# Kernel optimization log

Measured on AMD Instinct MI355X. Metric: run time of the kernel, lower is better.

The kernel has to match this reference:

```python
import jax, jax.numpy as jnp
import numpy as np

THRESHOLD = 0.4
MARGIN = 1.0
EPS = 1e-8  # torch F.cosine_similarity norm clamp


def setup_inputs() -> dict:
    key = jax.random.key(0)
    ks = jax.random.split(key, 8)
    B, N, D, T = 4096, 200000, 256, 10
    h_graph = jax.random.normal(ks[0], (B, D), jnp.float32)
    h_sub = jax.random.normal(ks[1], (N, D), jnp.float32)
    sub2graph = jax.random.randint(ks[2], (N,), 0, B, dtype=jnp.int32)
    W1 = jax.random.normal(ks[3], (D, 2 * D), jnp.float32) / np.float32(np.sqrt(D))
    b1 = jnp.zeros((2 * D,), jnp.float32)
    W2 = jax.random.normal(ks[4], (2 * D, 1), jnp.float32) / np.float32(np.sqrt(2 * D))
    b2 = jnp.zeros((1,), jnp.float32)
    Wc = jax.random.normal(ks[5], (2 * D, T), jnp.float32) / np.float32(np.sqrt(2 * D))
    bc = jnp.zeros((T,), jnp.float32)
    return dict(h_graph=h_graph, h_sub=h_sub, W1=W1, b1=b1, W2=W2, b2=b2,
                Wc=Wc, bc=bc, sub2graph=sub2graph)


def _forward(h_graph, h_sub, W1, b1, W2, b2, Wc, bc, sub2graph):
    B = h_graph.shape[0]
    dt = h_sub.dtype
    # SubMaskGenerator: Linear -> ReLU -> (Dropout off, eval) -> Linear -> sigmoid
    subgraph_mask = jax.nn.sigmoid((jax.nn.relu(h_sub @ W1 + b1) @ W2 + b2)[:, 0])  # [N]
    valid = (subgraph_mask > THRESHOLD).astype(dt)               # mask > threshold
    envm = (subgraph_mask <= THRESHOLD - 0.1).astype(dt)         # mask <= threshold-0.1
    # threshold-masked per-graph mean scatter (aggr='mean')
    sum_v = jax.ops.segment_sum(h_sub * valid[:, None], sub2graph, num_segments=B)
    cnt_v = jax.ops.segment_sum(valid, sub2graph, num_segments=B)
    h_sub_aligned = sum_v / jnp.maximum(cnt_v, 1.0)[:, None]     # zeros when no valid subs
    sum_e = jax.ops.segment_sum(h_sub * envm[:, None], sub2graph, num_segments=B)
    cnt_e = jax.ops.segment_sum(envm, sub2graph, num_segments=B)
    h_sub_env = sum_e / jnp.maximum(cnt_e, 1.0)[:, None]
    # pairwise cosine distances (norms clamped like torch)
    an = jnp.maximum(jnp.linalg.norm(h_sub_aligned, axis=-1), EPS)  # [B]
    en = jnp.maximum(jnp.linalg.norm(h_sub_env, axis=-1), EPS)      # [B]
    pos_d = 1.0 - (h_sub_aligned @ h_sub_aligned.T) / (an[:, None] * an[None, :])  # [B,B]
    neg_d = 1.0 - (h_sub_aligned @ h_sub_env.T) / (an[:, None] * en[None, :])      # [B,B]
    nz_pos = jnp.any(h_sub_aligned != 0, axis=1)
    nz_neg = jnp.any(h_sub_env != 0, axis=1)
    pos_num = jnp.maximum(nz_pos.sum() - 1, 1).astype(dt)
    num_env = nz_neg.sum()
    negative = (neg_d * nz_neg[None, :].astype(dt)).sum(1) / jnp.maximum(num_env, 1).astype(dt)
    positive = pos_d.sum(1) / pos_num
    contrib = jax.nn.relu(positive - negative + MARGIN) * nz_pos.astype(dt) * (num_env > 0).astype(dt)
    contrastive_loss = contrib.sum() / B
    out = jnp.concatenate([h_graph, h_sub_aligned], axis=1) @ Wc + bc
    return out, contrastive_loss, subgraph_mask


def reference(h_graph, h_sub, W1, b1, W2, b2, Wc, bc, sub2graph):
    return _forward(h_graph, h_sub, W1, b1, W2, b2, Wc, bc, sub2graph)
```

## Files before the change

kernel.cpp:

```cpp
#include <hip/hip_runtime.h>

#define N_SUB 200000
#define N_GR  4096
#define DIM   256
#define HID   512
#define TCLS  10
#define MROWS 64
#define RCAP  16384
#define RMARG 1e-3f
#define NREP  128

typedef __attribute__((ext_vector_type(8))) short short8;
typedef __attribute__((ext_vector_type(4))) float f32x4;

__device__ __forceinline__ short bf16_rne(float x){
  unsigned u = __builtin_bit_cast(unsigned, x);
  unsigned r = (u + 0x7FFFu + ((u >> 16) & 1u)) >> 16;
  return (short)r;
}
__device__ __forceinline__ float bf16_to_f(short h){
  unsigned u = ((unsigned)(unsigned short)h) << 16;
  return __builtin_bit_cast(float, u);
}
__device__ __forceinline__ float wave_reduce(float v){
  #pragma unroll
  for (int d = 1; d < 64; d <<= 1) v += __shfl_xor(v, d, 64);
  return v;
}
__device__ __forceinline__ int a_gran(int mt, int mrow, int ks, int kgrp){
  return (((((mt*8 + ks)*4 + kgrp)*2 + (mrow>>3)) << 3)
          | ((mrow & 7) ^ ((ks & 3) << 1) ^ (kgrp & 1)));
}

__global__ __launch_bounds__(256) void bconv_kernel(const float* __restrict__ W1,
                                                    short* __restrict__ bth,
                                                    short* __restrict__ btl,
                                                    int* cnt_all, float* S32, float* Se32,
                                                    float* S, float* Se,
                                                    int* counters, float* loss_p, int* rcnt){
  const int i = blockIdx.x*256 + threadIdx.x;
  if (i < N_GR) cnt_all[i] = 0;
  if (i < NREP*DIM){ S32[i] = 0.f; Se32[i] = 0.f; }
  if (i < DIM){ S[i] = 0.f; Se[i] = 0.f; }
  if (i < 64) loss_p[i] = 0.f;
  if (i < 2) counters[i] = 0;
  if (i == 0) rcnt[0] = 0;
  const int k = i >> 9;
  const int j = i & 511;
  const float x = W1[i];
  const short h = bf16_rne(x);
  const short l = bf16_rne(x - bf16_to_f(h));
  const int nt = j >> 4, mrow = j & 15;
  const int ksg = k >> 5, kgrp = (k >> 3) & 3, kk = k & 7;
  const int lane = kgrp*16 + mrow;
  const size_t dst = (((size_t)(nt*8 + ksg)*64 + lane) << 3) + kk;
  bth[dst] = h;
  btl[dst] = l;
}

__global__ __launch_bounds__(1024) void mask_gemm(
    const float* __restrict__ hsub, const short* __restrict__ bth,
    const short* __restrict__ btl, const float* __restrict__ b1,
    const float* __restrict__ W2, const float* __restrict__ b2,
    const int* __restrict__ s2g, float* __restrict__ mask_out,
    int* __restrict__ cnt_all, int* __restrict__ rlist, int* __restrict__ rcnt)
{
  __shared__ short a_hi[16384];
  __shared__ short a_lo[16384];
  __shared__ float sred[1024];
  const int tid = threadIdx.x;
  const int lane = tid & 63;
  const int c = tid >> 6;
  const int mrow = lane & 15;
  const int kgrp = lane >> 4;
  const int brow = blockIdx.x*MROWS;

  f32x4 acc[4][2];
  #pragma unroll
  for (int mt=0; mt<4; ++mt)
    #pragma unroll
    for (int nt=0; nt<2; ++nt) acc[mt][nt] = (f32x4){0.f,0.f,0.f,0.f};

  const float* __restrict__ gbase = hsub + (size_t)brow*DIM;
  {
    float4 g[4];
    #pragma unroll
    for (int i = 0; i < 4; ++i){
      const int idx = i*1024 + tid;
      g[i] = *reinterpret_cast<const float4*>(gbase + (size_t)idx*4);
    }
    #pragma unroll
    for (int i = 0; i < 4; ++i){
      const int idx = i*1024 + tid;
      const int rr = idx >> 6;
      const int ch = idx & 63;
      const float4 v = g[i];
      const short h0=bf16_rne(v.x), h1=bf16_rne(v.y), h2=bf16_rne(v.z), h3=bf16_rne(v.w);
      const short l0=bf16_rne(v.x-bf16_to_f(h0)), l1=bf16_rne(v.y-bf16_to_f(h1));
      const short l2=bf16_rne(v.z-bf16_to_f(h2)), l3=bf16_rne(v.w-bf16_to_f(h3));
      const int so = a_gran(rr>>4, rr&15, ch>>3, (ch>>1)&3)*8 + (ch&1)*4;
      *reinterpret_cast<short4*>(&a_hi[so]) = make_short4(h0,h1,h2,h3);
      *reinterpret_cast<short4*>(&a_lo[so]) = make_short4(l0,l1,l2,l3);
    }
  }
  __syncthreads();

  short8 Ah[4], Al[4];
  #pragma unroll
  for (int ks = 0; ks < 8; ++ks){
    #pragma unroll
    for (int m = 0; m < 4; ++m){
      const int so = a_gran(m, mrow, ks, kgrp)*8;
      Ah[m] = *reinterpret_cast<const short8*>(&a_hi[so]);
      Al[m] = *reinterpret_cast<const short8*>(&a_lo[so]);
    }
    #pragma unroll
    for (int nt = 0; nt < 2; ++nt){
      const int ntg = c*2 + nt;
      const size_t bo = (((size_t)(ntg*8 + ks)*64 + lane) << 3);
      const short8 Bh = *reinterpret_cast<const short8*>(bth + bo);
      const short8 Bl = *reinterpret_cast<const short8*>(btl + bo);
      #pragma unroll
      for (int m = 0; m < 4; ++m){
        acc[m][nt] = __builtin_amdgcn_mfma_f32_16x16x32_bf16(Ah[m], Bh, acc[m][nt], 0,0,0);
        acc[m][nt] = __builtin_amdgcn_mfma_f32_16x16x32_bf16(Ah[m], Bl, acc[m][nt], 0,0,0);
        acc[m][nt] = __builtin_amdgcn_mfma_f32_16x16x32_bf16(Al[m], Bh, acc[m][nt], 0,0,0);
      }
    }
  }

  float w2v[2], b1v[2];
  #pragma unroll
  for (int nt=0; nt<2; ++nt){
    const int n = c*32 + nt*16 + mrow;
    w2v[nt] = W2[n]; b1v[nt] = b1[n];
  }
  #pragma unroll
  for (int mt=0; mt<4; ++mt){
    #pragma unroll
    for (int r=0; r<4; ++r){
      float s = 0.f;
      #pragma unroll
      for (int nt=0; nt<2; ++nt)
        s += fmaxf(acc[mt][nt][r] + b1v[nt], 0.f) * w2v[nt];
      s += __shfl_xor(s, 1, 64);
      s += __shfl_xor(s, 2, 64);
      s += __shfl_xor(s, 4, 64);
      s += __shfl_xor(s, 8, 64);
      if (mrow == 0)
        sred[c*64 + mt*16 + kgrp*4 + r] = s;
    }
  }
  __syncthreads();
  if (tid < MROWS){
    const int rr = brow + tid;
    float tot = b2[0];
    #pragma unroll
    for (int w = 0; w < 16; ++w) tot += sred[w*64 + tid];
    const float m = 1.f / (1.f + expf(-tot));
    mask_out[rr] = m;
    atomicAdd(&cnt_all[s2g[rr]], 1);
    if (fabsf(m - 0.4f) < RMARG || fabsf(m - 0.3f) < RMARG){
      const int p = atomicAdd(rcnt, 1);
      if (p < RCAP) rlist[p] = rr;
    }
  }
}

__global__ __launch_bounds__(512) void refine_kernel(
    const float* __restrict__ hsub, const float* __restrict__ W1,
    const float* __restrict__ b1, const float* __restrict__ W2,
    const float* __restrict__ b2, const int* __restrict__ rlist,
    const int* __restrict__ rcnt, float* __restrict__ mask_out)
{
  __shared__ float arow[256];
  __shared__ float red[512];
  const int n = min(rcnt[0], RCAP);
  const int t = threadIdx.x;
  for (int it = blockIdx.x; it < n; it += gridDim.x){
    const int row = rlist[it];
    if (t < 256) arow[t] = hsub[(size_t)row*DIM + t];
    __syncthreads();
    float y0 = b1[t], y1 = 0.f, y2 = 0.f, y3 = 0.f;
    #pragma unroll 8
    for (int k = 0; k < 64; ++k){
      y0 = fmaf(arow[k],     W1[(size_t)k*512 + t],         y0);
      y1 = fmaf(arow[k+64],  W1[(size_t)(k+64)*512 + t],    y1);
      y2 = fmaf(arow[k+128], W1[(size_t)(k+128)*512 + t],   y2);
      y3 = fmaf(arow[k+192], W1[(size_t)(k+192)*512 + t],   y3);
    }
    const float y = (y0 + y1) + (y2 + y3);
    red[t] = fmaxf(y, 0.f) * W2[t];
    __syncthreads();
    #pragma unroll
    for (int off = 256; off > 0; off >>= 1){
      if (t < off) red[t] += red[t+off];
      __syncthreads();
    }
    if (t == 0) mask_out[row] = 1.f / (1.f + expf(-(red[0] + b2[0])));
    __syncthreads();
  }
}

__global__ __launch_bounds__(1024) void scan_kernel(const int* __restrict__ cnt,
                                                    int* __restrict__ offs,
                                                    int* __restrict__ cursor){
  __shared__ int buf[1024];
  const int t = threadIdx.x;
  const int c0 = cnt[t*4], c1 = cnt[t*4+1], c2 = cnt[t*4+2], c3 = cnt[t*4+3];
  const int s = c0+c1+c2+c3;
  buf[t] = s; __syncthreads();
  for (int d = 1; d < 1024; d <<= 1){
    int v = (t >= d) ? buf[t-d] : 0;
    __syncthreads();
    buf[t] += v;
    __syncthreads();
  }
  const int excl = buf[t] - s;
  const int o0 = excl, o1 = excl+c0, o2 = o1+c1, o3 = o2+c2;
  offs[t*4]=o0; offs[t*4+1]=o1; offs[t*4+2]=o2; offs[t*4+3]=o3;
  cursor[t*4]=o0; cursor[t*4+1]=o1; cursor[t*4+2]=o2; cursor[t*4+3]=o3;
  if (t == 1023) offs[4096] = buf[1023];
}

__global__ void fill_kernel(const int* __restrict__ s2g, int* __restrict__ cursor,
                            int* __restrict__ list){
  const int i = blockIdx.x*blockDim.x + threadIdx.x;
  if (i < N_SUB){
    const int g = s2g[i];
    const int p = atomicAdd(&cursor[g], 1);
    list[p] = i;
  }
}

__global__ __launch_bounds__(256) void graph_means(
    const float* __restrict__ hsub, const float* __restrict__ mask,
    const int* __restrict__ list, const int* __restrict__ offs,
    const float* __restrict__ hgraph, const float* __restrict__ Wc,
    const float* __restrict__ bc, unsigned short* __restrict__ hatAb,
    float* __restrict__ S32, float* __restrict__ Se32,
    int* __restrict__ nzflags, int* __restrict__ counters,
    float* __restrict__ out)
{
  __shared__ int   sidx[256];
  __shared__ unsigned char sflag[256];
  __shared__ float wr4[4][4];
  __shared__ float wrc[TCLS][4];
  const int g = blockIdx.x;
  const int t = threadIdx.x;
  const int w = t >> 6, lane = t & 63;
  const int start = offs[g], end = offs[g+1];
  const int cnt = end - start;
  float sv = 0.f, sev = 0.f;
  int cv = 0, ce = 0;
  for (int base = 0; base < cnt; base += 256){
    const int nb = min(256, cnt - base);
    __syncthreads();
    if (t < nb){
      const int i = list[start + base + t];
      sidx[t] = i;
      const float m = mask[i];
      sflag[t] = (m > 0.4f) ? 1 : ((m <= 0.3f) ? 2 : 0);
    }
    __syncthreads();
    for (int p = 0; p < nb; p += 4){
      const int lim = nb - p;
      const int i0 = sidx[p];
      const int i1 = (lim > 1) ? sidx[p+1] : i0;
      const int i2 = (lim > 2) ? sidx[p+2] : i0;
      const int i3 = (lim > 3) ? sidx[p+3] : i0;
      const int f0 = sflag[p];
      const int f1 = (lim > 1) ? sflag[p+1] : 0;
      const int f2 = (lim > 2) ? sflag[p+2] : 0;
      const int f3 = (lim > 3) ? sflag[p+3] : 0;
      const float v0 = hsub[(size_t)i0*DIM + t];
      const float v1 = hsub[(size_t)i1*DIM + t];
      const float v2 = hsub[(size_t)i2*DIM + t];
      const float v3 = hsub[(size_t)i3*DIM + t];
      if (f0==1){ sv+=v0; cv++; } else if (f0==2){ sev+=v0; ce++; }
      if (f1==1){ sv+=v1; cv++; } else if (f1==2){ sev+=v1; ce++; }
      if (f2==1){ sv+=v2; cv++; } else if (f2==2){ sev+=v2; ce++; }
      if (f3==1){ sv+=v3; cv++; } else if (f3==2){ sev+=v3; ce++; }
    }
  }
  __syncthreads();
  const float aligned = sv  / fmaxf((float)cv, 1.f);
  const float envv    = sev / fmaxf((float)ce, 1.f);
  float r0 = wave_reduce(aligned*aligned);
  float r1 = wave_reduce(envv*envv);
  float r2 = wave_reduce(aligned != 0.f ? 1.f : 0.f);
  float r3 = wave_reduce(envv    != 0.f ? 1.f : 0.f);
  if (lane == 0){ wr4[w][0]=r0; wr4[w][1]=r1; wr4[w][2]=r2; wr4[w][3]=r3; }
  __syncthreads();
  const float an2  = wr4[0][0]+wr4[1][0]+wr4[2][0]+wr4[3][0];
  const float en2  = wr4[0][1]+wr4[1][1]+wr4[2][1]+wr4[3][1];
  const float nzpf = wr4[0][2]+wr4[1][2]+wr4[2][2]+wr4[3][2];
  const float nzef = wr4[0][3]+wr4[1][3]+wr4[2][3]+wr4[3][3];
  const bool nzp = nzpf > 0.f, nze = nzef > 0.f;
  const float an = fmaxf(sqrtf(an2), 1e-8f);
  const float en = fmaxf(sqrtf(en2), 1e-8f);
  const float ha = aligned / an;
  hatAb[(size_t)g*DIM + t] = (unsigned short)bf16_rne(ha);
  atomicAdd(&S32[((g & (NREP-1)) << 8) + t], ha);
  if (nze) atomicAdd(&Se32[((g & (NREP-1)) << 8) + t], envv / en);
  if (t == 0){
    nzflags[g] = nzp ? 1 : 0;
    if (nzp) atomicAdd(&counters[0], 1);
    if (nze) atomicAdd(&counters[1], 1);
  }
  const float hg = hgraph[(size_t)g*DIM + t];
  #pragma unroll
  for (int c = 0; c < TCLS; ++c){
    float part = hg*Wc[t*TCLS+c] + aligned*Wc[(DIM+t)*TCLS+c];
    part = wave_reduce(part);
    if (lane == 0) wrc[c][w] = part;
  }
  __syncthreads();
  if (t < TCLS)
    out[g*TCLS + t] = wrc[t][0]+wrc[t][1]+wrc[t][2]+wrc[t][3] + bc[t];
}

__global__ __launch_bounds__(256) void combine_kernel(const float* __restrict__ S32,
                                                      const float* __restrict__ Se32,
                                                      float* __restrict__ S,
                                                      float* __restrict__ Se){
  const int b = blockIdx.x;
  const int t = threadIdx.x;
  float s = 0.f, se = 0.f;
  #pragma unroll
  for (int r = 0; r < 8; ++r){
    s  += S32[(b*8 + r)*DIM + t];
    se += Se32[(b*8 + r)*DIM + t];
  }
  atomicAdd(&S[t], s);
  atomicAdd(&Se[t], se);
}

__global__ __launch_bounds__(256) void loss_kernel(
    const unsigned short* __restrict__ hatAb, const float* __restrict__ S,
    const float* __restrict__ Se, const int* __restrict__ nzflags,
    const int* __restrict__ counters, float* __restrict__ loss_p)
{
  __shared__ float wr[4][2];
  const int g = blockIdx.x, t = threadIdx.x;
  const int w = t >> 6, lane = t & 63;
  const float ha = bf16_to_f((short)hatAb[(size_t)g*DIM + t]);
  float p0 = wave_reduce(ha*S[t]);
  float p1 = wave_reduce(ha*Se[t]);
  if (lane == 0){ wr[w][0] = p0; wr[w][1] = p1; }
  __syncthreads();
  if (t == 0){
    const float dS  = wr[0][0]+wr[1][0]+wr[2][0]+wr[3][0];
    const float dSe = wr[0][1]+wr[1][1]+wr[2][1]+wr[3][1];
    const int nzp_cnt = counters[0];
    const int nenv = counters[1];
    const float pos_num = fmaxf((float)(nzp_cnt - 1), 1.f);
    const float positive = (4096.f - dS) / pos_num;
    const float negative = ((float)nenv - dSe) / fmaxf((float)nenv, 1.f);
    float contrib = fmaxf(positive - negative + 1.f, 0.f);
    contrib *= (nzflags[g] ? 1.f : 0.f) * ((nenv > 0) ? 1.f : 0.f);
    atomicAdd(&loss_p[g & 63], contrib * (1.f/4096.f));
  }
}

__global__ void final_loss(const float* __restrict__ loss_p, float* __restrict__ loss){
  const int t = threadIdx.x;
  float v = loss_p[t];
  v = wave_reduce(v);
  if (t == 0) loss[0] = v;
}

extern "C" void kernel_launch(void* const* d_in, const int* in_sizes, int n_in,
                              void* d_out, int out_size, void* d_ws, size_t ws_size,
                              hipStream_t stream) {
  const float* h_graph = (const float*)d_in[0];
  const float* h_sub   = (const float*)d_in[1];
  const float* W1      = (const float*)d_in[2];
  const float* b1      = (const float*)d_in[3];
  const float* W2      = (const float*)d_in[4];
  const float* b2      = (const float*)d_in[5];
  const float* Wc      = (const float*)d_in[6];
  const float* bc      = (const float*)d_in[7];
  const int*   s2g     = (const int*)d_in[8];

  float* out  = (float*)d_out;
  float* loss = out + N_GR*TCLS;
  float* mask = loss + 1;

  char* ws = (char*)d_ws;
  short* bth    = (short*)ws;
  short* btl    = bth + HID*DIM;
  unsigned short* hatAb = (unsigned short*)(btl + HID*DIM);
  int* cnt_all  = (int*)(hatAb + (size_t)N_GR*DIM);
  int* offs     = cnt_all + N_GR;
  int* cursor   = offs + N_GR + 1;
  int* list     = cursor + N_GR;
  int* nzflags  = list + N_SUB;
  int* counters = nzflags + N_GR;
  int* rcnt     = counters + 2;
  int* rlist    = rcnt + 1;
  float* S      = (float*)(rlist + RCAP);
  float* Se     = S + DIM;
  float* S32    = Se + DIM;
  float* Se32   = S32 + NREP*DIM;
  float* loss_p = Se32 + NREP*DIM;

  hipLaunchKernelGGL(bconv_kernel, dim3(HID*DIM/256), dim3(256), 0, stream,
                     W1, bth, btl, cnt_all, S32, Se32, S, Se, counters, loss_p, rcnt);
  hipLaunchKernelGGL(mask_gemm, dim3(N_SUB/MROWS), dim3(1024), 0, stream,
                     h_sub, bth, btl, b1, W2, b2, s2g, mask, cnt_all, rlist, rcnt);
  hipLaunchKernelGGL(refine_kernel, dim3(384), dim3(512), 0, stream,
                     h_sub, W1, b1, W2, b2, rlist, rcnt, mask);
  hipLaunchKernelGGL(scan_kernel, dim3(1), dim3(1024), 0, stream,
                     cnt_all, offs, cursor);
  hipLaunchKernelGGL(fill_kernel, dim3((N_SUB+255)/256), dim3(256), 0, stream,
                     s2g, cursor, list);
  hipLaunchKernelGGL(graph_means, dim3(N_GR), dim3(256), 0, stream,
                     h_sub, mask, list, offs, h_graph, Wc, bc,
                     hatAb, S32, Se32, nzflags, counters, out);
  hipLaunchKernelGGL(combine_kernel, dim3(16), dim3(256), 0, stream,
                     S32, Se32, S, Se);
  hipLaunchKernelGGL(loss_kernel, dim3(N_GR), dim3(256), 0, stream,
                     hatAb, S, Se, nzflags, counters, loss_p);
  hipLaunchKernelGGL(final_loss, dim3(1), dim3(64), 0, stream,
                     loss_p, loss);
}
```

Baseline: 398.2 us.

## Process two row tiles per mask_gemm block with prefetched second-tile loads

Each mask_gemm block now handles two 64-row tiles. Global loads for both tiles are issued up front, so the second tile's fetch overlaps the first tile's conversion, MFMA work and epilogue. The aim is to hide HBM latency and halve the block count, at the cost of holding extra registers for the prefetched data and serialising the two tiles within a block. Bounds clamping is added for the odd final tile.

Result: slower. 408.5 us (+2.6%).

```diff
diff --git a/kernel.cpp b/kernel.cpp
--- a/kernel.cpp
+++ b/kernel.cpp
@@ -73,98 +73,123 @@
   const int c = tid >> 6;
   const int mrow = lane & 15;
   const int kgrp = lane >> 4;
-  const int brow = blockIdx.x*MROWS;
+  const int brow1 = blockIdx.x*(2*MROWS);
+  const int brow2 = brow1 + MROWS;
 
   f32x4 acc[4][2];
+
+#define CONVERT(G)                                                            \
+  { _Pragma("unroll")                                                         \
+    for (int i = 0; i < 4; ++i){                                              \
+      const int idx = i*1024 + tid;                                           \
+      const int rr = idx >> 6;                                                \
+      const int ch = idx & 63;                                                \
+      const float4 v = G[i];                                                  \
+      const short h0=bf16_rne(v.x), h1=bf16_rne(v.y), h2=bf16_rne(v.z), h3=bf16_rne(v.w); \
+      const short l0=bf16_rne(v.x-bf16_to_f(h0)), l1=bf16_rne(v.y-bf16_to_f(h1)); \
+      const short l2=bf16_rne(v.z-bf16_to_f(h2)), l3=bf16_rne(v.w-bf16_to_f(h3)); \
+      const int so = a_gran(rr>>4, rr&15, ch>>3, (ch>>1)&3)*8 + (ch&1)*4;     \
+      *reinterpret_cast<short4*>(&a_hi[so]) = make_short4(h0,h1,h2,h3);       \
+      *reinterpret_cast<short4*>(&a_lo[so]) = make_short4(l0,l1,l2,l3);       \
+    } }
+
+#define KSLOOP                                                                \
+  { short8 Ah[4], Al[4];                                                      \
+    _Pragma("unroll")                                                         \
+    for (int ks = 0; ks < 8; ++ks){                                           \
+      _Pragma("unroll")                                                       \
+      for (int m = 0; m < 4; ++m){                                            \
+        const int so = a_gran(m, mrow, ks, kgrp)*8;                           \
+        Ah[m] = *reinterpret_cast<const short8*>(&a_hi[so]);                  \
+        Al[m] = *reinterpret_cast<const short8*>(&a_lo[so]);                  \
+      }                                                                       \
+      _Pragma("unroll")                                                       \
+      for (int nt = 0; nt < 2; ++nt){                                         \
+        const int ntg = c*2 + nt;                                             \
+        const size_t bo = (((size_t)(ntg*8 + ks)*64 + lane) << 3);            \
+        const short8 Bh = *reinterpret_cast<const short8*>(bth + bo);         \
+        const short8 Bl = *reinterpret_cast<const short8*>(btl + bo);         \
+        _Pragma("unroll")                                                     \
+        for (int m = 0; m < 4; ++m){                                          \
+          acc[m][nt] = __builtin_amdgcn_mfma_f32_16x16x32_bf16(Ah[m], Bh, acc[m][nt], 0,0,0); \
+          acc[m][nt] = __builtin_amdgcn_mfma_f32_16x16x32_bf16(Ah[m], Bl, acc[m][nt], 0,0,0); \
+          acc[m][nt] = __builtin_amdgcn_mfma_f32_16x16x32_bf16(Al[m], Bh, acc[m][nt], 0,0,0); \
+        } } } }
+
+#define EPILOGUE(BROW)                                                        \
+  { float w2v[2], b1v[2];                                                     \
+    _Pragma("unroll")                                                         \
+    for (int nt=0; nt<2; ++nt){                                               \
+      const int n = c*32 + nt*16 + mrow;                                      \
+      w2v[nt] = W2[n]; b1v[nt] = b1[n];                                       \
+    }                                                                         \
+    _Pragma("unroll")                                                         \
+    for (int mt=0; mt<4; ++mt){                                               \
+      _Pragma("unroll")                                                       \
+      for (int r=0; r<4; ++r){                                                \
+        float s = 0.f;                                                        \
+        _Pragma("unroll")                                                     \
+        for (int nt=0; nt<2; ++nt)                                            \
+          s += fmaxf(acc[mt][nt][r] + b1v[nt], 0.f) * w2v[nt];                \
+        s += __shfl_xor(s, 1, 64);                                            \
+        s += __shfl_xor(s, 2, 64);                                            \
+        s += __shfl_xor(s, 4, 64);                                            \
+        s += __shfl_xor(s, 8, 64);                                            \
+        if (mrow == 0)                                                        \
+          sred[c*64 + mt*16 + kgrp*4 + r] = s;                                \
+      } }                                                                     \
+    __syncthreads();                                                          \
+    if (tid < MROWS){                                                         \
+      const int rr = (BROW) + tid;                                            \
+      if (rr < N_SUB){                                                        \
+        float tot = b2[0];                                                    \
+        _Pragma("unroll")                                                     \
+        for (int w = 0; w < 16; ++w) tot += sred[w*64 + tid];                 \
+        const float m = 1.f / (1.f + expf(-tot));                             \
+        mask_out[rr] = m;                                                     \
+        atomicAdd(&cnt_all[s2g[rr]], 1);                                      \
+        if (fabsf(m - 0.4f) < RMARG || fabsf(m - 0.3f) < RMARG){              \
+          const int p = atomicAdd(rcnt, 1);                                   \
+          if (p < RCAP) rlist[p] = rr;                                        \
+        }                                                                     \
+      } } }
+
+  float4 g1[4], g2[4];
+  #pragma unroll
+  for (int i = 0; i < 4; ++i){
+    const int idx = i*1024 + tid;
+    g1[i] = *reinterpret_cast<const float4*>(hsub + (size_t)(brow1 + (idx>>6))*DIM + (idx&63)*4);
+  }
+  #pragma unroll
+  for (int i = 0; i < 4; ++i){
+    const int idx = i*1024 + tid;
+    const int rg = min(brow2 + (idx>>6), N_SUB-1);
+    g2[i] = *reinterpret_cast<const float4*>(hsub + (size_t)rg*DIM + (idx&63)*4);
+  }
+
   #pragma unroll
   for (int mt=0; mt<4; ++mt)
     #pragma unroll
     for (int nt=0; nt<2; ++nt) acc[mt][nt] = (f32x4){0.f,0.f,0.f,0.f};
-
-  const float* __restrict__ gbase = hsub + (size_t)brow*DIM;
-  {
-    float4 g[4];
+  CONVERT(g1);
+  __syncthreads();
+  KSLOOP;
+  EPILOGUE(brow1);
+  __syncthreads();
+
+  if (brow2 < N_SUB){
     #pragma unroll
-    for (int i = 0; i < 4; ++i){
-      const int idx = i*1024 + tid;
-      g[i] = *reinterpret_cast<const float4*>(gbase + (size_t)idx*4);
-    }
-    #pragma unroll
-    for (int i = 0; i < 4; ++i){
-      const int idx = i*1024 + tid;
-      const int rr = idx >> 6;
-      const int ch = idx & 63;
-      const float4 v = g[i];
-      const short h0=bf16_rne(v.x), h1=bf16_rne(v.y), h2=bf16_rne(v.z), h3=bf16_rne(v.w);
-      const short l0=bf16_rne(v.x-bf16_to_f(h0)), l1=bf16_rne(v.y-bf16_to_f(h1));
-      const short l2=bf16_rne(v.z-bf16_to_f(h2)), l3=bf16_rne(v.w-bf16_to_f(h3));
-      const int so = a_gran(rr>>4, rr&15, ch>>3, (ch>>1)&3)*8 + (ch&1)*4;
-      *reinterpret_cast<short4*>(&a_hi[so]) = make_short4(h0,h1,h2,h3);
-      *reinterpret_cast<short4*>(&a_lo[so]) = make_short4(l0,l1,l2,l3);
-    }
-  }
-  __syncthreads();
-
-  short8 Ah[4], Al[4];
-  #pragma unroll
-  for (int ks = 0; ks < 8; ++ks){
-    #pragma unroll
-    for (int m = 0; m < 4; ++m){
-      const int so = a_gran(m, mrow, ks, kgrp)*8;
-      Ah[m] = *reinterpret_cast<const short8*>(&a_hi[so]);
-      Al[m] = *reinterpret_cast<const short8*>(&a_lo[so]);
-    }
-    #pragma unroll
-    for (int nt = 0; nt < 2; ++nt){
-      const int ntg = c*2 + nt;
-      const size_t bo = (((size_t)(ntg*8 + ks)*64 + lane) << 3);
-      const short8 Bh = *reinterpret_cast<const short8*>(bth + bo);
-      const short8 Bl = *reinterpret_cast<const short8*>(btl + bo);
+    for (int mt=0; mt<4; ++mt)
       #pragma unroll
-      for (int m = 0; m < 4; ++m){
-        acc[m][nt] = __builtin_amdgcn_mfma_f32_16x16x32_bf16(Ah[m], Bh, acc[m][nt], 0,0,0);
-        acc[m][nt] = __builtin_amdgcn_mfma_f32_16x16x32_bf16(Ah[m], Bl, acc[m][nt], 0,0,0);
-        acc[m][nt] = __builtin_amdgcn_mfma_f32_16x16x32_bf16(Al[m], Bh, acc[m][nt], 0,0,0);
-      }
-    }
-  }
-
-  float w2v[2], b1v[2];
-  #pragma unroll
-  for (int nt=0; nt<2; ++nt){
-    const int n = c*32 + nt*16 + mrow;
-    w2v[nt] = W2[n]; b1v[nt] = b1[n];
-  }
-  #pragma unroll
-  for (int mt=0; mt<4; ++mt){
-    #pragma unroll
-    for (int r=0; r<4; ++r){
-      float s = 0.f;
-      #pragma unroll
-      for (int nt=0; nt<2; ++nt)
-        s += fmaxf(acc[mt][nt][r] + b1v[nt], 0.f) * w2v[nt];
-      s += __shfl_xor(s, 1, 64);
-      s += __shfl_xor(s, 2, 64);
-      s += __shfl_xor(s, 4, 64);
-      s += __shfl_xor(s, 8, 64);
-      if (mrow == 0)
-        sred[c*64 + mt*16 + kgrp*4 + r] = s;
-    }
-  }
-  __syncthreads();
-  if (tid < MROWS){
-    const int rr = brow + tid;
-    float tot = b2[0];
-    #pragma unroll
-    for (int w = 0; w < 16; ++w) tot += sred[w*64 + tid];
-    const float m = 1.f / (1.f + expf(-tot));
-    mask_out[rr] = m;
-    atomicAdd(&cnt_all[s2g[rr]], 1);
-    if (fabsf(m - 0.4f) < RMARG || fabsf(m - 0.3f) < RMARG){
-      const int p = atomicAdd(rcnt, 1);
-      if (p < RCAP) rlist[p] = rr;
-    }
-  }
+      for (int nt=0; nt<2; ++nt) acc[mt][nt] = (f32x4){0.f,0.f,0.f,0.f};
+    CONVERT(g2);
+    __syncthreads();
+    KSLOOP;
+    EPILOGUE(brow2);
+  }
+#undef CONVERT
+#undef KSLOOP
+#undef EPILOGUE
 }
 
 __global__ __launch_bounds__(512) void refine_kernel(
@@ -407,7 +432,7 @@
 
   hipLaunchKernelGGL(bconv_kernel, dim3(HID*DIM/256), dim3(256), 0, stream,
                      W1, bth, btl, cnt_all, S32, Se32, S, Se, counters, loss_p, rcnt);
-  hipLaunchKernelGGL(mask_gemm, dim3(N_SUB/MROWS), dim3(1024), 0, stream,
+  hipLaunchKernelGGL(mask_gemm, dim3((N_SUB + 2*MROWS - 1)/(2*MROWS)), dim3(1024), 0, stream,
                      h_sub, bth, btl, b1, W2, b2, s2g, mask, cnt_all, rlist, rcnt);
   hipLaunchKernelGGL(refine_kernel, dim3(384), dim3(512), 0, stream,
                      h_sub, W1, b1, W2, b2, rlist, rcnt, mask);
```
